# Performance work log

Measured on AMD Instinct MI355X. Metric: run time of the kernel, lower is better.

The kernel has to match this reference:

```python
import jax, jax.numpy as jnp
import numpy as np

HIDDEN_DIM = 64
VOCAB_SIZE = 64
MEMORY_SLOTS = 4
SEQ_LEN = 48
B = 524288


def setup_inputs() -> dict:
    key = jax.random.key(0)
    ks = jax.random.split(key, 6)
    seqs = jax.random.randint(ks[0], (B, SEQ_LEN), 0, VOCAB_SIZE, dtype=jnp.int64 if jax.config.jax_enable_x64 else jnp.int32)
    query_tok = jax.random.randint(ks[1], (B,), 0, VOCAB_SIZE, dtype=seqs.dtype)
    embed = jax.random.normal(ks[2], (VOCAB_SIZE + 2, HIDDEN_DIM), dtype=jnp.float32) * 0.02
    W1 = jax.random.normal(ks[3], (HIDDEN_DIM, HIDDEN_DIM * 2), dtype=jnp.float32) * 0.05
    b1 = jnp.zeros((HIDDEN_DIM,), dtype=jnp.float32)
    W2 = jax.random.normal(ks[4], (VOCAB_SIZE, HIDDEN_DIM), dtype=jnp.float32) * 0.05
    b2 = jnp.zeros((VOCAB_SIZE,), dtype=jnp.float32)
    return {"seqs": seqs, "query_tok": query_tok, "embed": embed,
            "W1": W1, "b1": b1, "W2": W2, "b2": b2}


def reference(seqs, query_tok, embed, W1, b1, W2, b2):
    # FIFO of size MEMORY_SLOTS over tokens t=0..SEQ_LEN-2 == last MEMORY_SLOTS of them
    mem_tok = seqs[:, SEQ_LEN - 1 - MEMORY_SLOTS:SEQ_LEN - 1]      # [B, MEMORY_SLOTS]
    mem_summary = embed[mem_tok].mean(axis=1)                       # [B, H]
    q_emb = embed[query_tok]                                        # [B, H]
    x = jnp.concatenate([q_emb, mem_summary], axis=-1)              # [B, 2H]
    h = jax.nn.relu(x @ W1.T + b1)                                  # [B, H]
    return h @ W2.T + b2                                            # [B, VOCAB]
```

## Files before the change

kernel.cpp:

```cpp
#include <hip/hip_runtime.h>
#include <hip/hip_bf16.h>

#define HD 64
#define VOCAB 64
#define SEQ 48
#define MEMSLOTS 4
#define TSTRIDE 66

using frag_ab = __attribute__((ext_vector_type(8))) short;
using frag_cd = __attribute__((ext_vector_type(4))) float;
typedef __attribute__((ext_vector_type(4))) float floatx4;

static __device__ inline unsigned short f2bf(float f) {
  unsigned u = __float_as_uint(f);
  unsigned r = (u + 0x7fffu + ((u >> 16) & 1u)) >> 16;
  return (unsigned short)r;
}

__global__ void build_tables(const float* __restrict__ embed,
                             const float* __restrict__ W1,
                             const float* __restrict__ b1,
                             float* __restrict__ T) {
  int v = blockIdx.x;
  int j = threadIdx.x;
  const float* e = embed + v * HD;
  const float* w1r = W1 + j * (2 * HD);
  float s1 = 0.f, s2 = 0.f;
  for (int k = 0; k < HD; ++k) {
    float ev = e[k];
    s1 += ev * w1r[k];
    s2 += ev * w1r[HD + k];
  }
  T[v * TSTRIDE + j] = s1 + b1[j];
  T[VOCAB * TSTRIDE + v * TSTRIDE + j] = 0.25f * s2;
}

__global__ __launch_bounds__(256, 4) void lru_main(
    const int* __restrict__ seqs, const int* __restrict__ qtok,
    const float* __restrict__ W2, const float* __restrict__ b2,
    const float* __restrict__ T, float* __restrict__ out, int nbatch) {
  __shared__ float sT[2 * VOCAB * TSTRIDE];

  {
    const floatx4* src = (const floatx4*)T;
    floatx4* dst = (floatx4*)sT;
    const int n4 = 2 * VOCAB * TSTRIDE / 4;
    for (int i = threadIdx.x; i < n4; i += blockDim.x) dst[i] = src[i];
  }
  __syncthreads();

  const int lane = threadIdx.x & 63;
  const int quad = lane >> 4;
  const int m    = lane & 15;
  const int k0   = quad * 8;

  frag_ab bf[4][2];
  for (int t = 0; t < 4; ++t)
    for (int s = 0; s < 2; ++s) {
      const float* w2r = W2 + (t * 16 + m) * HD + s * 32 + k0;
      for (int j = 0; j < 8; ++j) bf[t][s][j] = (short)f2bf(w2r[j]);
    }
  float b2v[4];
  for (int t = 0; t < 4; ++t) b2v[t] = b2[t * 16 + m];

  const int wave = blockIdx.x * (blockDim.x >> 6) + (threadIdx.x >> 6);
  const int nw   = gridDim.x * (blockDim.x >> 6);

  const float* T1 = sT;
  const float* T2 = sT + VOCAB * TSTRIDE;

  for (int b = wave; b < nbatch; b += nw) {
    const int rb  = b * 16;
    const int row = rb + m;
    const int q   = qtok[row];
    const int* sp = seqs + row * SEQ;
    const int ta  = sp[43];
    const int4 tb = *(const int4*)(sp + 44);

    float2 a[8];
    {
      const float2* p1  = (const float2*)(T1 + q * TSTRIDE + k0);
      const float2* p1b = (const float2*)(T1 + q * TSTRIDE + 32 + k0);
      for (int c = 0; c < 4; ++c) { a[c] = p1[c]; a[4 + c] = p1b[c]; }
      const int toks[4] = {ta, tb.x, tb.y, tb.z};
      for (int u = 0; u < 4; ++u) {
        const float2* p2  = (const float2*)(T2 + toks[u] * TSTRIDE + k0);
        const float2* p2b = (const float2*)(T2 + toks[u] * TSTRIDE + 32 + k0);
        for (int c = 0; c < 4; ++c) {
          float2 x = p2[c], y = p2b[c];
          a[c].x += x.x; a[c].y += x.y;
          a[4 + c].x += y.x; a[4 + c].y += y.y;
        }
      }
    }

    frag_ab a0, a1;
    for (int c = 0; c < 4; ++c) {
      a0[2 * c]     = (short)f2bf(fmaxf(a[c].x, 0.f));
      a0[2 * c + 1] = (short)f2bf(fmaxf(a[c].y, 0.f));
      a1[2 * c]     = (short)f2bf(fmaxf(a[4 + c].x, 0.f));
      a1[2 * c + 1] = (short)f2bf(fmaxf(a[4 + c].y, 0.f));
    }

    frag_cd acc[4];
    for (int t = 0; t < 4; ++t) {
      acc[t] = (frag_cd){0.f, 0.f, 0.f, 0.f};
      acc[t] = __builtin_amdgcn_mfma_f32_16x16x32_bf16(a0, bf[t][0], acc[t], 0, 0, 0);
      acc[t] = __builtin_amdgcn_mfma_f32_16x16x32_bf16(a1, bf[t][1], acc[t], 0, 0, 0);
    }

    float* orow = out + (size_t)rb * HD;
    for (int t = 0; t < 4; ++t)
      for (int p = 0; p < 4; ++p)
        orow[(quad * 4 + p) * HD + t * 16 + m] = acc[t][p] + b2v[t];
  }
}

extern "C" void kernel_launch(void* const* d_in, const int* in_sizes, int n_in,
                              void* d_out, int out_size, void* d_ws, size_t ws_size,
                              hipStream_t stream) {
  const int*   seqs  = (const int*)d_in[0];
  const int*   qtok  = (const int*)d_in[1];
  const float* embed = (const float*)d_in[2];
  const float* W1    = (const float*)d_in[3];
  const float* b1    = (const float*)d_in[4];
  const float* W2    = (const float*)d_in[5];
  const float* b2    = (const float*)d_in[6];
  float* out = (float*)d_out;
  float* T   = (float*)d_ws;

  const int B = in_sizes[1];
  const int nbatch = B / 16;

  build_tables<<<VOCAB, HD, 0, stream>>>(embed, W1, b1, T);
  lru_main<<<2048, 256, 0, stream>>>(seqs, qtok, W2, b2, T, out, nbatch);
}
```

Before: 238.6 us.

## Swap MFMA operands for row-contiguous float4 stores and vectorize table reads

Swaps the MFMA A/B operands so each lane holds four consecutive output columns of one batch row. This lets results be written as float4 stores instead of scattered scalar stores, and the bias is loaded as float4 to match. The table stride becomes 68 so shared-memory reads can use 16-byte floatx4 loads, and bf16 conversion now uses a packed intrinsic. The cost is a slightly larger LDS table and possible bank-conflict changes from the new stride.

```diff
diff --git a/kernel.cpp b/kernel.cpp
--- a/kernel.cpp
+++ b/kernel.cpp
@@ -5,7 +5,7 @@
 #define VOCAB 64
 #define SEQ 48
 #define MEMSLOTS 4
-#define TSTRIDE 66
+#define TSTRIDE 68
 
 using frag_ab = __attribute__((ext_vector_type(8))) short;
 using frag_cd = __attribute__((ext_vector_type(4))) float;
@@ -15,6 +15,14 @@
   unsigned u = __float_as_uint(f);
   unsigned r = (u + 0x7fffu + ((u >> 16) & 1u)) >> 16;
   return (unsigned short)r;
+}
+
+static __device__ inline unsigned pack_bf16(float lo, float hi) {
+  float2 f2 = make_float2(lo, hi);
+  __hip_bfloat162 h2 = __float22bfloat162_rn(f2);
+  unsigned u;
+  __builtin_memcpy(&u, &h2, 4);
+  return u;
 }
 
 __global__ void build_tables(const float* __restrict__ embed,
@@ -54,14 +62,15 @@
   const int m    = lane & 15;
   const int k0   = quad * 8;
 
-  frag_ab bf[4][2];
+  frag_ab af[4][2];
   for (int t = 0; t < 4; ++t)
     for (int s = 0; s < 2; ++s) {
       const float* w2r = W2 + (t * 16 + m) * HD + s * 32 + k0;
-      for (int j = 0; j < 8; ++j) bf[t][s][j] = (short)f2bf(w2r[j]);
+      for (int j = 0; j < 8; ++j) af[t][s][j] = (short)f2bf(w2r[j]);
     }
-  float b2v[4];
-  for (int t = 0; t < 4; ++t) b2v[t] = b2[t * 16 + m];
+  floatx4 b2q[4];
+  for (int t = 0; t < 4; ++t)
+    b2q[t] = *(const floatx4*)(b2 + t * 16 + quad * 4);
 
   const int wave = blockIdx.x * (blockDim.x >> 6) + (threadIdx.x >> 6);
   const int nw   = gridDim.x * (blockDim.x >> 6);
@@ -77,42 +86,50 @@
     const int ta  = sp[43];
     const int4 tb = *(const int4*)(sp + 44);
 
-    float2 a[8];
+    floatx4 v0, v1, v2, v3;
     {
-      const float2* p1  = (const float2*)(T1 + q * TSTRIDE + k0);
-      const float2* p1b = (const float2*)(T1 + q * TSTRIDE + 32 + k0);
-      for (int c = 0; c < 4; ++c) { a[c] = p1[c]; a[4 + c] = p1b[c]; }
+      const floatx4* p1 = (const floatx4*)(T1 + q * TSTRIDE + k0);
+      v0 = p1[0]; v1 = p1[1]; v2 = p1[8]; v3 = p1[9];
       const int toks[4] = {ta, tb.x, tb.y, tb.z};
+#pragma unroll
       for (int u = 0; u < 4; ++u) {
-        const float2* p2  = (const float2*)(T2 + toks[u] * TSTRIDE + k0);
-        const float2* p2b = (const float2*)(T2 + toks[u] * TSTRIDE + 32 + k0);
-        for (int c = 0; c < 4; ++c) {
-          float2 x = p2[c], y = p2b[c];
-          a[c].x += x.x; a[c].y += x.y;
-          a[4 + c].x += y.x; a[4 + c].y += y.y;
-        }
+        const floatx4* p2 = (const floatx4*)(T2 + toks[u] * TSTRIDE + k0);
+        v0 += p2[0]; v1 += p2[1]; v2 += p2[8]; v3 += p2[9];
       }
     }
 
-    frag_ab a0, a1;
+#pragma unroll
     for (int c = 0; c < 4; ++c) {
-      a0[2 * c]     = (short)f2bf(fmaxf(a[c].x, 0.f));
-      a0[2 * c + 1] = (short)f2bf(fmaxf(a[c].y, 0.f));
-      a1[2 * c]     = (short)f2bf(fmaxf(a[4 + c].x, 0.f));
-      a1[2 * c + 1] = (short)f2bf(fmaxf(a[4 + c].y, 0.f));
+      v0[c] = fmaxf(v0[c], 0.f);
+      v1[c] = fmaxf(v1[c], 0.f);
+      v2[c] = fmaxf(v2[c], 0.f);
+      v3[c] = fmaxf(v3[c], 0.f);
     }
 
+    union { frag_ab v; unsigned u[4]; } A0, A1;
+    A0.u[0] = pack_bf16(v0[0], v0[1]);
+    A0.u[1] = pack_bf16(v0[2], v0[3]);
+    A0.u[2] = pack_bf16(v1[0], v1[1]);
+    A0.u[3] = pack_bf16(v1[2], v1[3]);
+    A1.u[0] = pack_bf16(v2[0], v2[1]);
+    A1.u[1] = pack_bf16(v2[2], v2[3]);
+    A1.u[2] = pack_bf16(v3[0], v3[1]);
+    A1.u[3] = pack_bf16(v3[2], v3[3]);
+
     frag_cd acc[4];
+#pragma unroll
     for (int t = 0; t < 4; ++t) {
       acc[t] = (frag_cd){0.f, 0.f, 0.f, 0.f};
-      acc[t] = __builtin_amdgcn_mfma_f32_16x16x32_bf16(a0, bf[t][0], acc[t], 0, 0, 0);
-      acc[t] = __builtin_amdgcn_mfma_f32_16x16x32_bf16(a1, bf[t][1], acc[t], 0, 0, 0);
+      acc[t] = __builtin_amdgcn_mfma_f32_16x16x32_bf16(af[t][0], A0.v, acc[t], 0, 0, 0);
+      acc[t] = __builtin_amdgcn_mfma_f32_16x16x32_bf16(af[t][1], A1.v, acc[t], 0, 0, 0);
     }
 
-    float* orow = out + (size_t)rb * HD;
-    for (int t = 0; t < 4; ++t)
-      for (int p = 0; p < 4; ++p)
-        orow[(quad * 4 + p) * HD + t * 16 + m] = acc[t][p] + b2v[t];
+    float* orow = out + (size_t)(rb + m) * HD;
+#pragma unroll
+    for (int t = 0; t < 4; ++t) {
+      floatx4 o = acc[t] + b2q[t];
+      *(floatx4*)(orow + t * 16 + quad * 4) = o;
+    }
   }
 }
 
```

Result: no change. 239.9 us (+0.5%).
